# Kernel tuning notes

Hardware: AMD Instinct MI355X
Metric: run time of the kernel (lower is better)

## Reference

```python
import jax, jax.numpy as jnp
import numpy as np

SEQ, BATCH, D_MODEL, HEADS = 2048, 4, 1024, 16
D_K = D_MODEL // HEADS
SCALE = 1.0 / np.sqrt(D_K).astype(np.float32)


def setup_inputs() -> dict:
    key = jax.random.key(0)
    ks = jax.random.split(key, 12)
    s = 0.02
    inp = {
        "query": jax.random.normal(ks[0], (SEQ, BATCH, D_MODEL), jnp.float32),
        "key": jax.random.normal(ks[1], (SEQ, BATCH, D_MODEL), jnp.float32),
        "value": jax.random.normal(ks[2], (SEQ, BATCH, D_MODEL), jnp.float32),
        # causal mask [seq_q, seq_k, 1]; batch dim broadcasts per prepare_mask
        "mask": jnp.tril(jnp.ones((SEQ, SEQ), jnp.int32))[:, :, None],
        "Wq": jax.random.normal(ks[3], (D_MODEL, D_MODEL), jnp.float32) * s,
        "bq": jnp.zeros((D_MODEL,), jnp.float32),
        "Wk": jax.random.normal(ks[4], (D_MODEL, D_MODEL), jnp.float32) * s,
        "bk": jnp.zeros((D_MODEL,), jnp.float32),
        "Wv": jax.random.normal(ks[5], (D_MODEL, D_MODEL), jnp.float32) * s,
        "bv": jnp.zeros((D_MODEL,), jnp.float32),
        "Wo": jax.random.normal(ks[6], (D_MODEL, D_MODEL), jnp.float32) * s,
        "bo": jnp.zeros((D_MODEL,), jnp.float32),
    }
    return inp


def _heads(x, W, b):
    # [s, b, d_model] -> [s, b, h, d_k]
    y = jnp.einsum('sbd,de->sbe', x, W.T) + b
    return y.reshape(x.shape[0], x.shape[1], HEADS, D_K)


def reference(query, key, value, mask, Wq, bq, Wk, bk, Wv, bv, Wo, bo):
    seq_len, batch_size, _ = query.shape
    q = _heads(query, Wq, bq)
    k = _heads(key, Wk, bk)
    v = _heads(value, Wv, bv)
    # scores [i, j, b, h]
    scores = jnp.einsum('ibhd,jbhd->ijbh', q, k) * SCALE
    m = mask[:, :, :, None]  # [sq, sk, b_or_1, 1]
    scores = jnp.where(m == 0, jnp.float32(-jnp.inf), scores)
    attn = jax.nn.softmax(scores, axis=1)  # softmax over key dim j
    x = jnp.einsum('ijbh,jbhd->ibhd', attn, v)
    x = x.reshape(seq_len, batch_size, D_MODEL)
    return jnp.einsum('sbd,de->sbe', x, Wo.T) + bo
```

## Files before the change

### kernel.cpp

```cpp
#include <hip/hip_runtime.h>
#include <hip/hip_bf16.h>

#define SEQ 2048
#define BATCH 4
#define DM 1024
#define HEADS 16
#define DK 64
#define NBH 64
#define SC_LOG2E (0.125f * 1.4426950408889634f)

typedef unsigned short u16;
typedef __attribute__((ext_vector_type(8))) short bf16x8;
typedef __attribute__((ext_vector_type(4))) float f32x4;

__device__ inline u16 f2bf(float f) {
    unsigned int u = __builtin_bit_cast(unsigned int, f);
    u += 0x7fffu + ((u >> 16) & 1u);
    return (u16)(u >> 16);
}
__device__ inline float fexp2(float x) {
    float r; asm("v_exp_f32 %0, %1" : "=v"(r) : "v"(x)); return r;
}
__device__ inline unsigned pkbf(float a, float b) {
    unsigned r; asm("v_cvt_pk_bf16_f32 %0, %1, %2" : "=v"(r) : "v"(a), "v"(b)); return r;
}

__global__ __launch_bounds__(256)
void conv_w(const float* __restrict__ wq, const float* __restrict__ wk,
            const float* __restrict__ wv, const float* __restrict__ wo,
            u16* __restrict__ ow)
{
    const size_t W8 = (size_t)DM * DM / 8;
    size_t i = (size_t)blockIdx.x * 256 + threadIdx.x;
    int wsel = (int)(i >> 17);
    size_t off = i & (W8 - 1);
    const float* src = wsel == 0 ? wq : wsel == 1 ? wk : wsel == 2 ? wv : wo;
    u16* dst = ow + (size_t)wsel * DM * DM;
    float4 a = ((const float4*)src)[off * 2];
    float4 b = ((const float4*)src)[off * 2 + 1];
    uint4 w;
    w.x = pkbf(a.x, a.y); w.y = pkbf(a.z, a.w);
    w.z = pkbf(b.x, b.y); w.w = pkbf(b.z, b.w);
    *(uint4*)(dst + off * 8) = w;
}

__device__ inline void gstage(const u16* __restrict__ src, u16* dst,
                              int wave, int lane) {
    #pragma unroll
    for (int i = 0; i < 4; ++i) {
        int ci = (i * 4 + wave) * 64 + lane;
        int row = ci >> 3, ch = ci & 7;
        const u16* g = src + (size_t)row * 1024 + ((ch ^ (row & 7)) << 3);
        u16* l = dst + (i * 4 + wave) * 512;
        __builtin_amdgcn_global_load_lds(
            (const __attribute__((address_space(1))) unsigned int*)g,
            (__attribute__((address_space(3))) unsigned int*)l, 16, 0, 0);
    }
}
__device__ inline bf16x8 rdt(const u16* t, int row, int ch) {
    return *(const bf16x8*)(t + row * 64 + ((ch ^ (row & 7)) << 3));
}

template<int MODE>
__device__ inline void gemm_epilogue(f32x4 acc[4][4], const float* bias,
                                     void* Out, float oscale,
                                     int row0, int col0, int wr, int wc,
                                     int lg, int l15) {
    #pragma unroll
    for (int m = 0; m < 4; ++m)
        #pragma unroll
        for (int n = 0; n < 4; ++n)
            #pragma unroll
            for (int r = 0; r < 4; ++r) {
                int R = row0 + wr + m * 16 + lg * 4 + r;
                int E = col0 + wc + n * 16 + l15;
                float v = (acc[m][n][r] + bias[E]) * oscale;
                if (MODE == 2) {
                    ((float*)Out)[(size_t)R * 1024 + E] = v;
                } else {
                    int s = R >> 2, b = R & 3, hh = E >> 6, d = E & 63;
                    size_t idx = (MODE == 0)
                        ? ((size_t)(b * HEADS + hh) * SEQ + s) * DK + d
                        : ((size_t)(b * HEADS + hh) * DK + d) * SEQ + s;
                    ((u16*)Out)[idx] = f2bf(v);
                }
            }
}

template<int MODE>
__global__ __launch_bounds__(256, 2)
void gemm_bf(const u16* __restrict__ A, const u16* __restrict__ B,
             const float* __restrict__ bias, void* __restrict__ Out, float oscale)
{
    __shared__ __align__(16) u16 sA[2][128 * 64];
    __shared__ __align__(16) u16 sB[2][128 * 64];
    const int tid  = threadIdx.x;
    const int lane = tid & 63, wave = tid >> 6;
    const int wr = (wave >> 1) * 64, wc = (wave & 1) * 64;
    const int l15 = lane & 15, lg = lane >> 4;
    const int row0 = blockIdx.x * 128, col0 = blockIdx.y * 128;
    const u16* Abase = A + (size_t)row0 * 1024;
    const u16* Bbase = B + (size_t)col0 * 1024;

    f32x4 acc[4][4];
    #pragma unroll
    for (int m = 0; m < 4; ++m)
        #pragma unroll
        for (int n = 0; n < 4; ++n) acc[m][n] = (f32x4){0.f, 0.f, 0.f, 0.f};

    gstage(Abase, sA[0], wave, lane);
    gstage(Bbase, sB[0], wave, lane);
    __syncthreads();

    int cur = 0;
    for (int kt = 0; kt < 16; ++kt) {
        if (kt < 15) {
            gstage(Abase + (kt + 1) * 64, sA[cur ^ 1], wave, lane);
            gstage(Bbase + (kt + 1) * 64, sB[cur ^ 1], wave, lane);
        }
        #pragma unroll
        for (int s = 0; s < 2; ++s) {
            bf16x8 af[4], bf[4];
            #pragma unroll
            for (int m = 0; m < 4; ++m)
                af[m] = rdt(sA[cur], wr + m * 16 + l15, s * 4 + lg);
            #pragma unroll
            for (int n = 0; n < 4; ++n)
                bf[n] = rdt(sB[cur], wc + n * 16 + l15, s * 4 + lg);
            __builtin_amdgcn_s_setprio(1);
            #pragma unroll
            for (int m = 0; m < 4; ++m)
                #pragma unroll
                for (int n = 0; n < 4; ++n)
                    acc[m][n] = __builtin_amdgcn_mfma_f32_16x16x32_bf16(
                        af[m], bf[n], acc[m][n], 0, 0, 0);
            __builtin_amdgcn_s_setprio(0);
        }
        __syncthreads();
        cur ^= 1;
    }
    gemm_epilogue<MODE>(acc, bias, Out, oscale, row0, col0, wr, wc, lg, l15);
}

template<int MODE>
__global__ __launch_bounds__(256, 2)
void gemm_af32(const float* __restrict__ A, const u16* __restrict__ B,
               const float* __restrict__ bias, void* __restrict__ Out, float oscale)
{
    __shared__ __align__(16) u16 sA[2][128 * 64];
    __shared__ __align__(16) u16 sB[2][128 * 64];
    const int tid  = threadIdx.x;
    const int lane = tid & 63, wave = tid >> 6;
    const int wr = (wave >> 1) * 64, wc = (wave & 1) * 64;
    const int l15 = lane & 15, lg = lane >> 4;
    const int row0 = blockIdx.x * 128, col0 = blockIdx.y * 128;
    const int arow = tid >> 4;
    const int ach  = tid & 15;
    const float* Ag = A + (size_t)(row0 + arow) * 1024 + ach * 4;
    const u16* Bbase = B + (size_t)col0 * 1024;

    f32x4 acc[4][4];
    #pragma unroll
    for (int m = 0; m < 4; ++m)
        #pragma unroll
        for (int n = 0; n < 4; ++n) acc[m][n] = (f32x4){0.f, 0.f, 0.f, 0.f};

    auto loadA = [&](int kt, float4* r) {
        #pragma unroll
        for (int i = 0; i < 8; ++i)
            r[i] = *(const float4*)(Ag + (size_t)i * 16 * 1024 + kt * 64);
    };
    auto writeA = [&](const float4* r, u16* dst) {
        const int c16 = ach >> 1, half = ach & 1;
        #pragma unroll
        for (int i = 0; i < 8; ++i) {
            int row = arow + 16 * i;
            uint2 w;
            w.x = pkbf(r[i].x, r[i].y);
            w.y = pkbf(r[i].z, r[i].w);
            *(uint2*)(dst + row * 64 + ((c16 ^ (row & 7)) << 3) + half * 4) = w;
        }
    };

    {
        float4 a0[8];
        loadA(0, a0);
        gstage(Bbase, sB[0], wave, lane);
        writeA(a0, sA[0]);
    }
    __syncthreads();

    int cur = 0;
    for (int kt = 0; kt < 16; ++kt) {
        float4 an[8];
        const bool pre = (kt < 15);
        if (pre) {
            loadA(kt + 1, an);
            gstage(Bbase + (kt + 1) * 64, sB[cur ^ 1], wave, lane);
        }
        #pragma unroll
        for (int s = 0; s < 2; ++s) {
            bf16x8 af[4], bf[4];
            #pragma unroll
            for (int m = 0; m < 4; ++m)
                af[m] = rdt(sA[cur], wr + m * 16 + l15, s * 4 + lg);
            #pragma unroll
            for (int n = 0; n < 4; ++n)
                bf[n] = rdt(sB[cur], wc + n * 16 + l15, s * 4 + lg);
            __builtin_amdgcn_s_setprio(1);
            #pragma unroll
            for (int m = 0; m < 4; ++m)
                #pragma unroll
                for (int n = 0; n < 4; ++n)
                    acc[m][n] = __builtin_amdgcn_mfma_f32_16x16x32_bf16(
                        af[m], bf[n], acc[m][n], 0, 0, 0);
            __builtin_amdgcn_s_setprio(0);
        }
        if (pre) writeA(an, sA[cur ^ 1]);
        __syncthreads();
        cur ^= 1;
    }
    gemm_epilogue<MODE>(acc, bias, Out, oscale, row0, col0, wr, wc, lg, l15);
}

__device__ inline void stage_tile(const u16* __restrict__ srcRow0, int srcStride,
                                  u16* tile, int wave, int lane) {
    #pragma unroll
    for (int i = 0; i < 2; ++i) {
        int row = wave * 16 + i * 8 + (lane >> 3);
        int chunk = (lane & 7) ^ (row & 7);
        const u16* g = srcRow0 + (size_t)row * srcStride + chunk * 8;
        u16* l = tile + (wave * 16 + i * 8) * 64;
        __builtin_amdgcn_global_load_lds(
            (const __attribute__((address_space(1))) unsigned int*)g,
            (__attribute__((address_space(3))) unsigned int*)l, 16, 0, 0);
    }
}
__device__ inline bf16x8 tread(const u16* tile, int row, int chunk) {
    return *(const bf16x8*)((const char*)tile + row * 128 + ((chunk ^ (row & 7)) << 4));
}

__global__ __launch_bounds__(256, 4)
void attn_fwd(const u16* __restrict__ Q, const u16* __restrict__ K,
              const u16* __restrict__ V, u16* __restrict__ X)
{
    __shared__ __align__(16) u16 sK[2][4096];
    __shared__ __align__(16) u16 sV[2][4096];
    __shared__ __align__(16) u16 plds[4][16 * 64];

    const int lin = blockIdx.x + 16 * blockIdx.y;
    const int xcd = lin & 7, ii = lin >> 3;
    const int bh  = (ii & 7) | (xcd << 3);
    const int tA  = ii >> 3;
    const int tB  = 31 - tA;
    const int b = bh >> 4, h = bh & 15;
    const int lane = threadIdx.x & 63, wave = threadIdx.x >> 6;
    const int l15 = lane & 15, lg = lane >> 4;
    const int qloc = wave * 16 + l15;
    const int swz = (l15 & 7) << 4;
    const u16* Qh = Q + (size_t)bh * SEQ * DK;
    const u16* Kh = K + (size_t)bh * SEQ * DK;
    const u16* Vh = V + (size_t)bh * SEQ * DK;

    const int qA = tA * 64 + wave * 16, qB = tB * 64 + wave * 16;
    const bf16x8 qfA0 = *(const bf16x8*)&Qh[(size_t)(qA + l15) * DK + lg * 8];
    const bf16x8 qfA1 = *(const bf16x8*)&Qh[(size_t)(qA + l15) * DK + 32 + lg * 8];
    const bf16x8 qfB0 = *(const bf16x8*)&Qh[(size_t)(qB + l15) * DK + lg * 8];
    const bf16x8 qfB1 = *(const bf16x8*)&Qh[(size_t)(qB + l15) * DK + 32 + lg * 8];

    f32x4 oA[4], oB[4];
    #pragma unroll
    for (int n = 0; n < 4; ++n) {
        oA[n] = (f32x4){0.f, 0.f, 0.f, 0.f};
        oB[n] = (f32x4){0.f, 0.f, 0.f, 0.f};
    }
    float lsA = 0.f, lsB = 0.f;
    u16* pw = &plds[wave][0];

    auto compute = [&](const u16* kt, const u16* vt,
                       const bf16x8& q0v, const bf16x8& q1v,
                       f32x4* o, float& ls, bool diag) {
        f32x4 sc[4];
        #pragma unroll
        for (int c = 0; c < 4; ++c) sc[c] = (f32x4){0.f, 0.f, 0.f, 0.f};

        __builtin_amdgcn_s_setprio(1);
        #pragma unroll
        for (int c = 0; c < 4; ++c) {
            bf16x8 k0 = tread(kt, 16 * c + l15, lg);
            bf16x8 k1 = tread(kt, 16 * c + l15, 4 + lg);
            sc[c] = __builtin_amdgcn_mfma_f32_16x16x32_bf16(k0, q0v, sc[c], 0, 0, 0);
            sc[c] = __builtin_amdgcn_mfma_f32_16x16x32_bf16(k1, q1v, sc[c], 0, 0, 0);
        }
        __builtin_amdgcn_s_setprio(0);

        #pragma unroll
        for (int c = 0; c < 4; ++c) {
            float p[4];
            #pragma unroll
            for (int r = 0; r < 4; ++r) {
                float e = fexp2(sc[c][r]);
                if (diag) {
                    int kl = 16 * c + 4 * lg + r;
                    e = (kl <= qloc) ? e : 0.f;
                }
                p[r] = e;
                ls += e;
            }
            uint2 w;
            w.x = pkbf(p[0], p[1]);
            w.y = pkbf(p[2], p[3]);
            *(uint2*)((char*)pw + l15 * 128 + ((32 * c + 8 * lg) ^ swz)) = w;
        }
        asm volatile("s_waitcnt lgkmcnt(0)" ::: "memory");
        __builtin_amdgcn_sched_barrier(0);
        bf16x8 pf0 = *(const bf16x8*)((const char*)pw + l15 * 128 + ((16 * lg) ^ swz));
        bf16x8 pf1 = *(const bf16x8*)((const char*)pw + l15 * 128 + ((64 + 16 * lg) ^ swz));

        __builtin_amdgcn_s_setprio(1);
        #pragma unroll
        for (int n = 0; n < 4; ++n) {
            bf16x8 v0 = tread(vt, 16 * n + l15, lg);
            bf16x8 v1 = tread(vt, 16 * n + l15, 4 + lg);
            o[n] = __builtin_amdgcn_mfma_f32_16x16x32_bf16(pf0, v0, o[n], 0, 0, 0);
            o[n] = __builtin_amdgcn_mfma_f32_16x16x32_bf16(pf1, v1, o[n], 0, 0, 0);
        }
        __builtin_amdgcn_s_setprio(0);
    };

    stage_tile(Kh, DK, sK[0], wave, lane);
    stage_tile(Vh, SEQ, sV[0], wave, lane);
    __syncthreads();

    const int nst = tB + 1;
    int cur = 0;
    for (int blk = 0; blk < nst; ++blk) {
        if (blk + 1 < nst) {
            stage_tile(Kh + (size_t)(blk + 1) * 64 * DK, DK, sK[cur ^ 1], wave, lane);
            stage_tile(Vh + (blk + 1) * 64, SEQ, sV[cur ^ 1], wave, lane);
        }
        if (blk <= tA)
            compute(sK[cur], sV[cur], qfA0, qfA1, oA, lsA, blk == tA);
        compute(sK[cur], sV[cur], qfB0, qfB1, oB, lsB, blk == tB);
        __syncthreads();
        cur ^= 1;
    }

    auto finish = [&](f32x4* o, float ls, int q0) {
        float tot = ls;
        tot += __shfl_xor(tot, 16, 64);
        tot += __shfl_xor(tot, 32, 64);
        float inv[4];
        #pragma unroll
        for (int r = 0; r < 4; ++r)
            inv[r] = 1.0f / __shfl(tot, lg * 4 + r, 64);
        #pragma unroll
        for (int n = 0; n < 4; ++n)
            #pragma unroll
            for (int r = 0; r < 4; ++r) {
                const int i = q0 + lg * 4 + r;
                X[((size_t)i * BATCH + b) * DM + h * DK + 16 * n + l15] =
                    f2bf(o[n][r] * inv[r]);
            }
    };
    finish(oA, lsA, qA);
    finish(oB, lsB, qB);
}

extern "C" void kernel_launch(void* const* d_in, const int* in_sizes, int n_in,
                              void* d_out, int out_size, void* d_ws, size_t ws_size,
                              hipStream_t stream) {
    const float* query = (const float*)d_in[0];
    const float* key   = (const float*)d_in[1];
    const float* value = (const float*)d_in[2];
    const float* Wq = (const float*)d_in[4];
    const float* bq = (const float*)d_in[5];
    const float* Wk = (const float*)d_in[6];
    const float* bk = (const float*)d_in[7];
    const float* Wv = (const float*)d_in[8];
    const float* bv = (const float*)d_in[9];
    const float* Wo = (const float*)d_in[10];
    const float* bo = (const float*)d_in[11];

    const size_t NELEM = (size_t)SEQ * BATCH * DM;
    const size_t WM    = (size_t)DM * DM;
    u16* Qb  = (u16*)d_ws;
    u16* Kb  = Qb + NELEM;
    u16* Vt  = Kb + NELEM;
    u16* Xb  = Vt + NELEM;
    u16* Wbf = Xb + NELEM;

    dim3 gg(64, 8), gb(256);
    hipLaunchKernelGGL(conv_w, dim3(2048), gb, 0, stream, Wq, Wk, Wv, Wo, Wbf);
    hipLaunchKernelGGL((gemm_af32<0>), gg, gb, 0, stream, query, Wbf,          bq, Qb, SC_LOG2E);
    hipLaunchKernelGGL((gemm_af32<0>), gg, gb, 0, stream, key,   Wbf + WM,     bk, Kb, 1.0f);
    hipLaunchKernelGGL((gemm_af32<1>), gg, gb, 0, stream, value, Wbf + 2 * WM, bv, Vt, 1.0f);
    hipLaunchKernelGGL(attn_fwd, dim3(16, NBH), gb, 0, stream, Qb, Kb, Vt, Xb);
    hipLaunchKernelGGL((gemm_bf<2>),   gg, gb, 0, stream, Xb, Wbf + 3 * WM, bo, (float*)d_out, 1.0f);
}
```

Baseline: 175.9 us.

## Feed softmax probabilities to PV MFMA directly from registers, dropping LDS round trip

The P tile no longer goes through a per-wave LDS buffer. The score accumulator's register layout is reused as the A operand of 16x16x16 bf16 MFMAs, and V is read in matching 4-element fragments. This removes LDS writes, an lgkmcnt wait and the reads for P, and frees LDS. The cost is twice as many MFMA instructions, since the smaller K=16 variant replaces K=32, plus more live registers holding V fragments, which may affect occupancy.

```diff
diff --git a/kernel.cpp b/kernel.cpp
--- a/kernel.cpp
+++ b/kernel.cpp
@@ -11,6 +11,7 @@
 
 typedef unsigned short u16;
 typedef __attribute__((ext_vector_type(8))) short bf16x8;
+typedef __attribute__((ext_vector_type(4))) short bf16x4;
 typedef __attribute__((ext_vector_type(4))) float f32x4;
 
 __device__ inline u16 f2bf(float f) {
@@ -23,6 +24,9 @@
 }
 __device__ inline unsigned pkbf(float a, float b) {
     unsigned r; asm("v_cvt_pk_bf16_f32 %0, %1, %2" : "=v"(r) : "v"(a), "v"(b)); return r;
+}
+__device__ inline void mfma16(f32x4& d, bf16x4 a, bf16x4 b) {
+    asm("v_mfma_f32_16x16x16_bf16 %0, %1, %2, %0" : "+v"(d) : "v"(a), "v"(b));
 }
 
 __global__ __launch_bounds__(256)
@@ -239,6 +243,11 @@
 __device__ inline bf16x8 tread(const u16* tile, int row, int chunk) {
     return *(const bf16x8*)((const char*)tile + row * 128 + ((chunk ^ (row & 7)) << 4));
 }
+__device__ inline bf16x4 vread(const u16* tile, int n, int c, int l15, int lg) {
+    int row = 16 * n + l15;
+    int off = row * 128 + (((2 * c + (lg >> 1)) ^ (l15 & 7)) << 4) + (lg & 1) * 8;
+    return *(const bf16x4*)((const char*)tile + off);
+}
 
 __global__ __launch_bounds__(256, 4)
 void attn_fwd(const u16* __restrict__ Q, const u16* __restrict__ K,
@@ -246,7 +255,6 @@
 {
     __shared__ __align__(16) u16 sK[2][4096];
     __shared__ __align__(16) u16 sV[2][4096];
-    __shared__ __align__(16) u16 plds[4][16 * 64];
 
     const int lin = blockIdx.x + 16 * blockIdx.y;
     const int xcd = lin & 7, ii = lin >> 3;
@@ -257,7 +265,6 @@
     const int lane = threadIdx.x & 63, wave = threadIdx.x >> 6;
     const int l15 = lane & 15, lg = lane >> 4;
     const int qloc = wave * 16 + l15;
-    const int swz = (l15 & 7) << 4;
     const u16* Qh = Q + (size_t)bh * SEQ * DK;
     const u16* Kh = K + (size_t)bh * SEQ * DK;
     const u16* Vh = V + (size_t)bh * SEQ * DK;
@@ -275,7 +282,6 @@
         oB[n] = (f32x4){0.f, 0.f, 0.f, 0.f};
     }
     float lsA = 0.f, lsB = 0.f;
-    u16* pw = &plds[wave][0];
 
     auto compute = [&](const u16* kt, const u16* vt,
                        const bf16x8& q0v, const bf16x8& q1v,
@@ -293,6 +299,13 @@
             sc[c] = __builtin_amdgcn_mfma_f32_16x16x32_bf16(k1, q1v, sc[c], 0, 0, 0);
         }
         __builtin_amdgcn_s_setprio(0);
+
+        bf16x4 vb[4][4];
+        #pragma unroll
+        for (int n = 0; n < 4; ++n)
+            #pragma unroll
+            for (int c = 0; c < 4; ++c)
+                vb[n][c] = vread(vt, n, c, l15, lg);
 
         #pragma unroll
         for (int c = 0; c < 4; ++c) {
@@ -310,22 +323,13 @@
             uint2 w;
             w.x = pkbf(p[0], p[1]);
             w.y = pkbf(p[2], p[3]);
-            *(uint2*)((char*)pw + l15 * 128 + ((32 * c + 8 * lg) ^ swz)) = w;
-        }
-        asm volatile("s_waitcnt lgkmcnt(0)" ::: "memory");
-        __builtin_amdgcn_sched_barrier(0);
-        bf16x8 pf0 = *(const bf16x8*)((const char*)pw + l15 * 128 + ((16 * lg) ^ swz));
-        bf16x8 pf1 = *(const bf16x8*)((const char*)pw + l15 * 128 + ((64 + 16 * lg) ^ swz));
-
-        __builtin_amdgcn_s_setprio(1);
-        #pragma unroll
-        for (int n = 0; n < 4; ++n) {
-            bf16x8 v0 = tread(vt, 16 * n + l15, lg);
-            bf16x8 v1 = tread(vt, 16 * n + l15, 4 + lg);
-            o[n] = __builtin_amdgcn_mfma_f32_16x16x32_bf16(pf0, v0, o[n], 0, 0, 0);
-            o[n] = __builtin_amdgcn_mfma_f32_16x16x32_bf16(pf1, v1, o[n], 0, 0, 0);
-        }
-        __builtin_amdgcn_s_setprio(0);
+            bf16x4 pa = __builtin_bit_cast(bf16x4, w);
+            __builtin_amdgcn_s_setprio(1);
+            #pragma unroll
+            for (int n = 0; n < 4; ++n)
+                mfma16(o[n], pa, vb[n][c]);
+            __builtin_amdgcn_s_setprio(0);
+        }
     };
 
     stage_tile(Kh, DK, sK[0], wave, lane);
```

Result: no change. 179.2 us (+1.8%).
